# Kernel tuning notes

Measured on AMD Instinct MI355X. Metric: run time of the kernel, lower is better.

## Reference

```python
import jax, jax.numpy as jnp
import numpy as np

HIDDEN = 1024       # LUKE-large hidden size
NUM_HEADS = 16
NUM_ENTITIES = 42   # entities per doc (segment count)
EMBED = 768
BLOCK = 64
OUT_EMBED = 768
NUM_CLASS = 97
PROJ = 128
NEG_INF = -1e30


def setup_inputs() -> dict:
    key = jax.random.key(0)
    ks = jax.random.split(key, 16)
    B, L, M, R = 4, 1024, 128, 512
    s = 0.02
    return {
        "seq_lhs": jax.random.normal(ks[0], (B, L, HIDDEN), jnp.float32),
        "ent_lhs": jax.random.normal(ks[1], (B, M, HIDDEN), jnp.float32),
        "ent_to_seq_attn": jax.random.uniform(ks[2], (B, NUM_HEADS, M, L), jnp.float32),
        "entity_id_labels": jax.random.randint(ks[3], (B, M), 0, NUM_ENTITIES, jnp.int32),
        "hts": jax.random.randint(ks[4], (B, R, 2), 0, NUM_ENTITIES, jnp.int32),
        "W_head": jax.random.normal(ks[5], (2 * HIDDEN, EMBED), jnp.float32) * s,
        "b_head": jnp.zeros((EMBED,), jnp.float32),
        "W_tail": jax.random.normal(ks[6], (2 * HIDDEN, EMBED), jnp.float32) * s,
        "b_tail": jnp.zeros((EMBED,), jnp.float32),
        "W_bil": jax.random.normal(ks[7], (EMBED * BLOCK, OUT_EMBED), jnp.float32) * s,
        "b_bil": jnp.zeros((OUT_EMBED,), jnp.float32),
        "W_cls": jax.random.normal(ks[8], (OUT_EMBED, NUM_CLASS), jnp.float32) * s,
        "b_cls": jnp.zeros((NUM_CLASS,), jnp.float32),
        "W_proj": jax.random.normal(ks[9], (OUT_EMBED, PROJ), jnp.float32) * s,
        "b_proj": jnp.zeros((PROJ,), jnp.float32),
    }


def _pool_doc(seq, ent, attn, labels, ht):
    # seq [L,D], ent [M,D], attn [H,M,L], labels [M] int, ht [R,2] int
    onehot = (labels[None, :] == jnp.arange(NUM_ENTITIES)[:, None])  # [E,M]
    counts = onehot.sum(1)                                            # [E]
    # segment logsumexp over mentions (count==1 reduces to identity, matching torch)
    scores = jnp.where(onehot[:, :, None], ent[None, :, :], NEG_INF)  # [E,M,D]
    lse = jax.scipy.special.logsumexp(scores, axis=1)                 # [E,D]
    ent_emb = jnp.where(counts[:, None] > 0, lse, 0.0)                # zeros for empty entities
    # segment mean of attention over mentions: [E,H,L]
    oh = onehot.astype(attn.dtype)
    attn_sum = jnp.einsum('em,hml->ehl', oh, attn)
    attn_mean = attn_sum / jnp.maximum(counts, 1).astype(attn.dtype)[:, None, None]
    hs = ent_emb[ht[:, 0]]            # [R,D]
    ts = ent_emb[ht[:, 1]]            # [R,D]
    ha = attn_mean[ht[:, 0]]          # [R,H,L]
    ta = attn_mean[ht[:, 1]]          # [R,H,L]
    hta = (ha * ta).mean(1)           # [R,L]
    hta = hta / (hta.sum(1, keepdims=True) + 1e-5)
    rel = jnp.einsum('ld,rl->rd', seq, hta)  # [R,D]
    return hs, ts, rel


def reference(seq_lhs, ent_lhs, ent_to_seq_attn, entity_id_labels, hts,
              W_head, b_head, W_tail, b_tail, W_bil, b_bil, W_cls, b_cls, W_proj, b_proj):
    hs, ts, rel = jax.vmap(_pool_doc)(seq_lhs, ent_lhs, ent_to_seq_attn, entity_id_labels, hts)
    D = seq_lhs.shape[-1]
    hs = hs.reshape(-1, D)
    ts = ts.reshape(-1, D)
    rel = rel.reshape(-1, D)
    h = jnp.tanh(jnp.concatenate([hs, rel], axis=1) @ W_head + b_head)  # [N,EMBED]
    t = jnp.tanh(jnp.concatenate([ts, rel], axis=1) @ W_tail + b_tail)  # [N,EMBED]
    nb = EMBED // BLOCK
    b1 = h.reshape(-1, nb, BLOCK)
    b2 = t.reshape(-1, nb, BLOCK)
    bl = (b1[:, :, :, None] * b2[:, :, None, :]).reshape(-1, EMBED * BLOCK)
    embeds = bl @ W_bil + b_bil
    class_logits = embeds @ W_cls + b_cls
    proj_logits = jnp.tanh(embeds @ W_proj + b_proj)
    return embeds, class_logits, proj_logits
```

## Files before the change

### kernel.cpp

```cpp
#include <hip/hip_runtime.h>
#include <hip/hip_bf16.h>
#include <math.h>

#define BB   4
#define LL   1024
#define MM   128
#define RR   512
#define HID  1024
#define NH   16
#define NE   42
#define EMB  768
#define NBK  12
#define NC   97
#define PJ   128
#define NROWS 2048
#define KTOT (NBK * 4096)

typedef __attribute__((ext_vector_type(8))) short short8;
typedef __attribute__((ext_vector_type(4))) float floatx4;
typedef unsigned short ushort;

__device__ __forceinline__ float bf2f(ushort u) {
    return __uint_as_float(((unsigned int)u) << 16);
}
__device__ __forceinline__ ushort f2bf(float f) {
    __hip_bfloat16 h = __float2bfloat16(f);
    return *reinterpret_cast<ushort*>(&h);
}
__device__ __forceinline__ void async16(void* lds_base_uniform, const void* gsrc) {
    __builtin_amdgcn_global_load_lds(
        (const __attribute__((address_space(1))) unsigned int*)gsrc,
        (__attribute__((address_space(3))) unsigned int*)lds_base_uniform,
        16, 0, 0);
}
__device__ __forceinline__ void stage_w(short (*wlds)[4096], int bn,
                                        const ushort* wsrc, size_t t,
                                        int w, int lane) {
    const ushort* ts = wsrc + t * 4096;
    async16((void*)&wlds[bn][w * 512],        ts + w * 512 + lane * 8);
    async16((void*)&wlds[bn][2048 + w * 512], ts + 2048 + w * 512 + lane * 8);
}

__global__ __launch_bounds__(128) void k_members(const int* __restrict__ labels,
                                                 int* __restrict__ counts,
                                                 int* __restrict__ members) {
    int b = blockIdx.x;
    __shared__ int cnt[NE];
    int tid = threadIdx.x;
    if (tid < NE) cnt[tid] = 0;
    __syncthreads();
    if (tid < MM) {
        int lab = labels[b * MM + tid];
        int pos = atomicAdd(&cnt[lab], 1);
        members[(b * NE + lab) * MM + pos] = tid;
    }
    __syncthreads();
    if (tid < NE) counts[b * NE + tid] = cnt[tid];
}

__global__ __launch_bounds__(256) void k_entemb(const float* __restrict__ ent,
                                                const int* __restrict__ counts,
                                                const int* __restrict__ members,
                                                ushort* __restrict__ entbf) {
    int be = blockIdx.x;
    int b  = be / NE;
    int c  = counts[be];
    int tid = threadIdx.x;
    if (c == 0) {
#pragma unroll
        for (int u = 0; u < 4; ++u)
            entbf[(size_t)be * HID + tid + u * 256] = 0;
        return;
    }
    const int* mem = members + be * MM;
    const float* base = ent + (size_t)b * MM * HID;
#pragma unroll
    for (int u = 0; u < 4; ++u) {
        int d = tid + u * 256;
        float mx = -3.0e38f;
        for (int k = 0; k < c; ++k) {
            float x = base[(size_t)mem[k] * HID + d];
            mx = fmaxf(mx, x);
        }
        float s = 0.0f;
        for (int k = 0; k < c; ++k) {
            float x = base[(size_t)mem[k] * HID + d];
            s += expf(x - mx);
        }
        entbf[(size_t)be * HID + d] = f2bf(logf(s) + mx);
    }
}

__global__ __launch_bounds__(256) void k_attnmean(const float* __restrict__ attn,
                                                  const int* __restrict__ counts,
                                                  const int* __restrict__ members,
                                                  float* __restrict__ am) {
    int be = blockIdx.x;
    int hh = blockIdx.y;
    int b  = be / NE;
    int c  = counts[be];
    const int* mem = members + be * MM;
    float inv = 1.0f / (float)((c > 0) ? c : 1);
    const float* abase = attn + ((size_t)(b * NH + hh)) * MM * LL;
    int tid = threadIdx.x;
#pragma unroll
    for (int u = 0; u < 4; ++u) {
        int l = tid + u * 256;
        float s = 0.0f;
        for (int k = 0; k < c; ++k) s += abase[(size_t)mem[k] * LL + l];
        am[((size_t)be * NH + hh) * LL + l] = s * inv;
    }
}

__global__ __launch_bounds__(256) void k_hta(const float* __restrict__ am,
                                             const int* __restrict__ hts,
                                             ushort* __restrict__ htabf) {
    int br = blockIdx.x;
    int b  = br >> 9;
    int e0 = hts[br * 2 + 0];
    int e1 = hts[br * 2 + 1];
    const float* a0 = am + ((size_t)(b * NE + e0)) * NH * LL;
    const float* a1 = am + ((size_t)(b * NE + e1)) * NH * LL;
    int tid = threadIdx.x;
    float v[4] = {0.f, 0.f, 0.f, 0.f};
    for (int hh = 0; hh < NH; ++hh) {
        const float* p0 = a0 + hh * LL;
        const float* p1 = a1 + hh * LL;
#pragma unroll
        for (int u = 0; u < 4; ++u) {
            int l = tid + u * 256;
            v[u] = fmaf(p0[l], p1[l], v[u]);
        }
    }
    float part = 0.f;
#pragma unroll
    for (int u = 0; u < 4; ++u) { v[u] *= (1.0f / 16.0f); part += v[u]; }
    __shared__ float red[256];
    red[tid] = part;
    __syncthreads();
    for (int s = 128; s > 0; s >>= 1) {
        if (tid < s) red[tid] += red[tid + s];
        __syncthreads();
    }
    float scale = 1.0f / (red[0] + 1e-5f);
#pragma unroll
    for (int u = 0; u < 4; ++u)
        htabf[(size_t)br * LL + tid + u * 256] = f2bf(v[u] * scale);
}

__global__ __launch_bounds__(256) void k_prepB(const float* __restrict__ src,
                                               ushort* __restrict__ dst,
                                               int K, int N, long srcStride) {
    long flat = (long)blockIdx.x * 256 + threadIdx.x;
    int lane = (int)(flat & 63);
    long rest = flat >> 6;
    int cg = (int)(rest & 3); rest >>= 2;
    int NK0 = K >> 5;
    int k0 = (int)(rest % NK0); rest /= NK0;
    int NCB = N >> 6;
    int cb = (int)(rest % NCB);
    int bt = (int)(rest / NCB);
    int col = cb * 64 + cg * 16 + (lane & 15);
    int k   = k0 * 32 + (lane >> 4) * 8;
    const float* s = src + (size_t)bt * srcStride + (size_t)k * N + col;
    short8 out;
#pragma unroll
    for (int e = 0; e < 8; ++e)
        out[e] = (short)f2bf(s[(size_t)e * N]);
    *(short8*)(dst + (size_t)flat * 8) = out;
}

__global__ __launch_bounds__(256) void k_rel_mfma(const ushort* __restrict__ htabf,
                                                  const ushort* __restrict__ seqprep,
                                                  ushort* __restrict__ relbf) {
    __shared__ __align__(16) short wlds[2][4096];
    const int b = blockIdx.z;
    const int tid = threadIdx.x, lane = tid & 63, w = tid >> 6;
    const int lan16 = lane & 15, lgrp = lane >> 4;
    const int row0 = blockIdx.x * 128, cb = blockIdx.y, col0 = cb * 64;
    const ushort* wsrc = seqprep + ((size_t)b * 16 + cb) * 32 * 2048;
    const ushort* aP[2];
#pragma unroll
    for (int rg = 0; rg < 2; ++rg) {
        int r = row0 + w * 32 + rg * 16 + lan16;
        aP[rg] = htabf + ((size_t)b * RR + r) * LL;
    }
    floatx4 acc[2][4];
#pragma unroll
    for (int rg = 0; rg < 2; ++rg)
#pragma unroll
        for (int cg = 0; cg < 4; ++cg)
            acc[rg][cg] = (floatx4){0.f, 0.f, 0.f, 0.f};

    stage_w(wlds, 0, wsrc, 0, w, lane);
    __syncthreads();
    int buf = 0;
    for (int it = 0; it < 16; ++it) {
        short8 afr[2][2];
#pragma unroll
        for (int rg = 0; rg < 2; ++rg)
#pragma unroll
            for (int ks = 0; ks < 2; ++ks)
                afr[rg][ks] = *(const short8*)(aP[rg] + it * 64 + ks * 32 + lgrp * 8);
        if (it < 15) stage_w(wlds, buf ^ 1, wsrc, it + 1, w, lane);
#pragma unroll
        for (int ks = 0; ks < 2; ++ks) {
            short8 bfr[4];
#pragma unroll
            for (int cg = 0; cg < 4; ++cg)
                bfr[cg] = *(const short8*)&wlds[buf][ks * 2048 + cg * 512 + lane * 8];
#pragma unroll
            for (int rg = 0; rg < 2; ++rg)
#pragma unroll
                for (int cg = 0; cg < 4; ++cg)
                    acc[rg][cg] = __builtin_amdgcn_mfma_f32_16x16x32_bf16(
                        afr[rg][ks], bfr[cg], acc[rg][cg], 0, 0, 0);
        }
        __syncthreads();
        buf ^= 1;
    }
#pragma unroll
    for (int rg = 0; rg < 2; ++rg)
#pragma unroll
        for (int cg = 0; cg < 4; ++cg)
#pragma unroll
            for (int q = 0; q < 4; ++q) {
                int rr = row0 + w * 32 + rg * 16 + lgrp * 4 + q;
                int cc = col0 + cg * 16 + lan16;
                relbf[((size_t)b * RR + rr) * HID + cc] = f2bf(acc[rg][cg][q]);
            }
}

__global__ __launch_bounds__(256) void k_ht_mfma(const ushort* __restrict__ entbf,
                                                 const ushort* __restrict__ relbf,
                                                 const int* __restrict__ hts,
                                                 const ushort* __restrict__ wprepH,
                                                 const ushort* __restrict__ wprepT,
                                                 const float* __restrict__ bH,
                                                 const float* __restrict__ bT,
                                                 ushort* __restrict__ hT,
                                                 ushort* __restrict__ tbf) {
    __shared__ __align__(16) short wlds[2][4096];
    const int z = blockIdx.z;
    const ushort* wp  = z ? wprepT : wprepH;
    const float* bias = z ? bT : bH;
    const int tid = threadIdx.x, lane = tid & 63, w = tid >> 6;
    const int lan16 = lane & 15, lgrp = lane >> 4;
    const int row0 = blockIdx.x * 128, cb = blockIdx.y, col0 = cb * 64;
    const ushort* wsrc = wp + (size_t)cb * 64 * 2048;
    const ushort* aE[2];
    const ushort* aR[2];
#pragma unroll
    for (int rg = 0; rg < 2; ++rg) {
        int r = row0 + w * 32 + rg * 16 + lan16;
        int b = r >> 9, rr = r & 511;
        int e = hts[(b * RR + rr) * 2 + z];
        aE[rg] = entbf + (size_t)(b * NE + e) * HID;
        aR[rg] = relbf + (size_t)r * HID;
    }
    floatx4 acc[2][4];
#pragma unroll
    for (int rg = 0; rg < 2; ++rg)
#pragma unroll
        for (int cg = 0; cg < 4; ++cg)
            acc[rg][cg] = (floatx4){0.f, 0.f, 0.f, 0.f};

    stage_w(wlds, 0, wsrc, 0, w, lane);
    __syncthreads();
    int buf = 0;
    for (int it = 0; it < 32; ++it) {
        short8 afr[2][2];
        const int kb = (it < 16) ? it * 64 : it * 64 - 1024;
#pragma unroll
        for (int rg = 0; rg < 2; ++rg) {
            const ushort* ap = (it < 16 ? aE[rg] : aR[rg]) + kb + lgrp * 8;
#pragma unroll
            for (int ks = 0; ks < 2; ++ks)
                afr[rg][ks] = *(const short8*)(ap + ks * 32);
        }
        if (it < 31) stage_w(wlds, buf ^ 1, wsrc, it + 1, w, lane);
#pragma unroll
        for (int ks = 0; ks < 2; ++ks) {
            short8 bfr[4];
#pragma unroll
            for (int cg = 0; cg < 4; ++cg)
                bfr[cg] = *(const short8*)&wlds[buf][ks * 2048 + cg * 512 + lane * 8];
#pragma unroll
            for (int rg = 0; rg < 2; ++rg)
#pragma unroll
                for (int cg = 0; cg < 4; ++cg)
                    acc[rg][cg] = __builtin_amdgcn_mfma_f32_16x16x32_bf16(
                        afr[rg][ks], bfr[cg], acc[rg][cg], 0, 0, 0);
        }
        __syncthreads();
        buf ^= 1;
    }
#pragma unroll
    for (int rg = 0; rg < 2; ++rg)
#pragma unroll
        for (int cg = 0; cg < 4; ++cg)
#pragma unroll
            for (int q = 0; q < 4; ++q) {
                int rr = row0 + w * 32 + rg * 16 + lgrp * 4 + q;
                int cc = col0 + cg * 16 + lan16;
                ushort v = f2bf(tanhf(acc[rg][cg][q] + bias[cc]));
                if (z == 0) hT[(size_t)cc * NROWS + rr] = v;
                else        tbf[(size_t)rr * EMB + cc] = v;
            }
}

__global__ __launch_bounds__(256, 2) void k_bilinear(const ushort* __restrict__ hT,
                                                     const ushort* __restrict__ tbf,
                                                     const ushort* __restrict__ wprep,
                                                     float* __restrict__ partials) {
    __shared__ __align__(16) ushort h_lds[64 * 256];
    __shared__ __align__(16) short  wlds[2][4096];

    const int tid  = threadIdx.x;
    const int lane = tid & 63;
    const int w    = tid >> 6;
    const int lan16 = lane & 15;
    const int lgrp  = lane >> 4;
    const int rb = blockIdx.x, cb = blockIdx.y, zz = blockIdx.z;
    const int nb0 = zz * 3;
    const int row0 = rb * 256;
    const int col0 = cb * 64;
    const int rbase = w * 64;
    const ushort* wsrc = wprep + (size_t)((cb * 12 + nb0) * 64) * 4096;

    floatx4 acc[4][4];
#pragma unroll
    for (int rg = 0; rg < 4; ++rg)
#pragma unroll
        for (int cg = 0; cg < 4; ++cg)
            acc[rg][cg] = (floatx4){0.f, 0.f, 0.f, 0.f};

    stage_w(wlds, 0, wsrc, 0, w, lane);
    int buf = 0;
    for (int nbi = 0; nbi < 3; ++nbi) {
        const int nb = nb0 + nbi;
#pragma unroll
        for (int c = 0; c < 8; ++c) {
            void* dst = (void*)&h_lds[c * 2048 + w * 512];
            const ushort* src = hT + (size_t)(nb * 64 + c * 8 + w * 2 + (lane >> 5)) * NROWS
                                   + row0 + (lane & 31) * 8;
            async16(dst, src);
        }
        float tf[4][2][8];
#pragma unroll
        for (int rg = 0; rg < 4; ++rg)
#pragma unroll
            for (int ks = 0; ks < 2; ++ks) {
                const ushort* tp = tbf + (size_t)(row0 + rbase + rg * 16 + lan16) * EMB
                                       + nb * 64 + ks * 32 + lgrp * 8;
                short8 raw = *(const short8*)tp;
#pragma unroll
                for (int e = 0; e < 8; ++e)
                    tf[rg][ks][e] = bf2f((ushort)raw[e]);
            }
        __syncthreads();

        for (int i = 0; i < 64; ++i) {
            const int t = nbi * 64 + i;
            if (t < 191) stage_w(wlds, buf ^ 1, wsrc, t + 1, w, lane);
            float hv[4];
#pragma unroll
            for (int rg = 0; rg < 4; ++rg)
                hv[rg] = bf2f(h_lds[i * 256 + rbase + rg * 16 + lan16]);
#pragma unroll
            for (int ks = 0; ks < 2; ++ks) {
                short8 bfr[4];
#pragma unroll
                for (int cg = 0; cg < 4; ++cg)
                    bfr[cg] = *(const short8*)&wlds[buf][ks * 2048 + cg * 512 + lane * 8];
#pragma unroll
                for (int rg = 0; rg < 4; ++rg) {
                    short8 afr;
#pragma unroll
                    for (int e = 0; e < 8; ++e)
                        afr[e] = (short)f2bf(hv[rg] * tf[rg][ks][e]);
#pragma unroll
                    for (int cg = 0; cg < 4; ++cg)
                        acc[rg][cg] = __builtin_amdgcn_mfma_f32_16x16x32_bf16(
                            afr, bfr[cg], acc[rg][cg], 0, 0, 0);
                }
            }
            __syncthreads();
            buf ^= 1;
        }
    }

    float* pbase = partials + (size_t)zz * NROWS * EMB;
#pragma unroll
    for (int rg = 0; rg < 4; ++rg)
#pragma unroll
        for (int cg = 0; cg < 4; ++cg)
#pragma unroll
            for (int q = 0; q < 4; ++q)
                pbase[(size_t)(row0 + rbase + rg * 16 + lgrp * 4 + q) * EMB
                      + col0 + cg * 16 + lan16] = acc[rg][cg][q];
}

__global__ __launch_bounds__(256) void k_redbias(const float* __restrict__ partials,
                                                 const float* __restrict__ bias,
                                                 float* __restrict__ embeds) {
    int idx = blockIdx.x * 256 + threadIdx.x;
    const float4* p4 = (const float4*)partials;
    float4 s = p4[idx];
#pragma unroll
    for (int zz = 1; zz < 4; ++zz) {
        float4 v = p4[(size_t)zz * (NROWS * EMB / 4) + idx];
        s.x += v.x; s.y += v.y; s.z += v.z; s.w += v.w;
    }
    float4 b = ((const float4*)bias)[idx % (EMB / 4)];
    s.x += b.x; s.y += b.y; s.z += b.z; s.w += b.w;
    ((float4*)embeds)[idx] = s;
}

__global__ __launch_bounds__(256) void k_wcomb(const float* __restrict__ Wc,
                                               const float* __restrict__ Wp,
                                               float* __restrict__ Wcomb) {
    int k = blockIdx.x;
    int c = threadIdx.x;
    float v = (c < NC) ? Wc[(size_t)k * NC + c]
                       : ((c < NC + PJ) ? Wp[(size_t)k * PJ + (c - NC)] : 0.0f);
    Wcomb[(size_t)k * 256 + c] = v;
}

__global__ __launch_bounds__(256) void k_cls(const float* __restrict__ embeds,
                                             const float* __restrict__ Wcomb,
                                             const float* __restrict__ bc,
                                             const float* __restrict__ bp,
                                             float* __restrict__ cls_out,
                                             float* __restrict__ proj_out) {
    __shared__ float As[16][68];
    __shared__ float Bs[16][68];
    int tid = threadIdx.x;
    int tx = tid & 15, ty = tid >> 4;
    int row0 = blockIdx.x * 64, col0 = blockIdx.y * 64;
    float acc[4][4] = {};
    for (int k0 = 0; k0 < EMB; k0 += 16) {
        {
            int kk4 = (tid & 3) << 2, m = tid >> 2;
            float4 va = *(const float4*)&embeds[(size_t)(row0 + m) * EMB + k0 + kk4];
            As[kk4 + 0][m] = va.x; As[kk4 + 1][m] = va.y;
            As[kk4 + 2][m] = va.z; As[kk4 + 3][m] = va.w;
        }
        {
            int n4 = (tid & 15) << 2, kk = tid >> 4;
            float4 vb = *(const float4*)&Wcomb[(size_t)(k0 + kk) * 256 + col0 + n4];
            *(float4*)&Bs[kk][n4] = vb;
        }
        __syncthreads();
#pragma unroll
        for (int kk = 0; kk < 16; ++kk) {
            float4 a4 = *(const float4*)&As[kk][ty << 2];
            float4 b4 = *(const float4*)&Bs[kk][tx << 2];
            float av[4] = {a4.x, a4.y, a4.z, a4.w};
            float bv[4] = {b4.x, b4.y, b4.z, b4.w};
#pragma unroll
            for (int q = 0; q < 4; ++q)
#pragma unroll
                for (int p = 0; p < 4; ++p)
                    acc[q][p] = fmaf(av[q], bv[p], acc[q][p]);
        }
        __syncthreads();
    }
#pragma unroll
    for (int q = 0; q < 4; ++q)
#pragma unroll
        for (int p = 0; p < 4; ++p) {
            int c = col0 + (tx << 2) + p;
            int r = row0 + (ty << 2) + q;
            if (c < NC) {
                cls_out[(size_t)r * NC + c] = acc[q][p] + bc[c];
            } else if (c < NC + PJ) {
                int pp = c - NC;
                proj_out[(size_t)r * PJ + pp] = tanhf(acc[q][p] + bp[pp]);
            }
        }
}

extern "C" void kernel_launch(void* const* d_in, const int* in_sizes, int n_in,
                              void* d_out, int out_size, void* d_ws, size_t ws_size,
                              hipStream_t stream) {
    const float* seq    = (const float*)d_in[0];
    const float* ent    = (const float*)d_in[1];
    const float* attn   = (const float*)d_in[2];
    const int*   labels = (const int*)d_in[3];
    const int*   hts    = (const int*)d_in[4];
    const float* W_head = (const float*)d_in[5];
    const float* b_head = (const float*)d_in[6];
    const float* W_tail = (const float*)d_in[7];
    const float* b_tail = (const float*)d_in[8];
    const float* W_bil  = (const float*)d_in[9];
    const float* b_bil  = (const float*)d_in[10];
    const float* W_cls  = (const float*)d_in[11];
    const float* b_cls  = (const float*)d_in[12];
    const float* W_proj = (const float*)d_in[13];
    const float* b_proj = (const float*)d_in[14];

    char* p = (char*)d_ws;
    auto alloc = [&](size_t bytes) {
        void* r = (void*)p;
        p += (bytes + 255) & ~(size_t)255;
        return r;
    };
    int*    counts   = (int*)alloc(256 * 4);
    int*    members  = (int*)alloc((size_t)BB * NE * MM * 4);
    ushort* entbf    = (ushort*)alloc((size_t)BB * NE * HID * 2);
    float*  am       = (float*)alloc((size_t)BB * NE * NH * LL * 4);
    ushort* htabf    = (ushort*)alloc((size_t)BB * RR * LL * 2);
    ushort* relbf    = (ushort*)alloc((size_t)NROWS * HID * 2);
    ushort* hT       = (ushort*)alloc((size_t)EMB * NROWS * 2);
    ushort* tbf      = (ushort*)alloc((size_t)NROWS * EMB * 2);
    ushort* wprepBil = (ushort*)alloc((size_t)KTOT * EMB * 2);
    ushort* wprepH   = (ushort*)alloc((size_t)2 * HID * EMB * 2);
    ushort* wprepT   = (ushort*)alloc((size_t)2 * HID * EMB * 2);
    ushort* seqprep  = (ushort*)alloc((size_t)BB * LL * HID * 2);
    float*  Wcomb    = (float*)alloc((size_t)EMB * 256 * 4);
    float*  partials = (float*)alloc((size_t)4 * NROWS * EMB * 4);

    float* embeds_out = (float*)d_out;
    float* cls_out    = embeds_out + NROWS * EMB;
    float* proj_out   = cls_out + NROWS * NC;

    hipLaunchKernelGGL(k_prepB, dim3((size_t)KTOT * EMB / 8 / 256), dim3(256), 0, stream,
                       W_bil, wprepBil, KTOT, EMB, 0L);
    hipLaunchKernelGGL(k_prepB, dim3(2 * HID * EMB / 8 / 256), dim3(256), 0, stream,
                       W_head, wprepH, 2 * HID, EMB, 0L);
    hipLaunchKernelGGL(k_prepB, dim3(2 * HID * EMB / 8 / 256), dim3(256), 0, stream,
                       W_tail, wprepT, 2 * HID, EMB, 0L);
    hipLaunchKernelGGL(k_prepB, dim3(BB * LL * HID / 8 / 256), dim3(256), 0, stream,
                       seq, seqprep, LL, HID, (long)LL * HID);
    hipLaunchKernelGGL(k_wcomb, dim3(EMB), dim3(256), 0, stream,
                       W_cls, W_proj, Wcomb);

    hipLaunchKernelGGL(k_members, dim3(BB), dim3(128), 0, stream,
                       labels, counts, members);
    hipLaunchKernelGGL(k_entemb, dim3(BB * NE), dim3(256), 0, stream,
                       ent, counts, members, entbf);
    hipLaunchKernelGGL(k_attnmean, dim3(BB * NE, NH), dim3(256), 0, stream,
                       attn, counts, members, am);
    hipLaunchKernelGGL(k_hta, dim3(BB * RR), dim3(256), 0, stream,
                       am, hts, htabf);

    hipLaunchKernelGGL(k_rel_mfma, dim3(RR / 128, HID / 64, BB), dim3(256), 0, stream,
                       htabf, seqprep, relbf);
    hipLaunchKernelGGL(k_ht_mfma, dim3(NROWS / 128, EMB / 64, 2), dim3(256), 0, stream,
                       entbf, relbf, hts, wprepH, wprepT, b_head, b_tail, hT, tbf);
    hipLaunchKernelGGL(k_bilinear, dim3(NROWS / 256, EMB / 64, 4), dim3(256), 0, stream,
                       hT, tbf, wprepBil, partials);
    hipLaunchKernelGGL(k_redbias, dim3(NROWS * EMB / 4 / 256), dim3(256), 0, stream,
                       partials, b_bil, embeds_out);
    hipLaunchKernelGGL(k_cls, dim3(NROWS / 64, 4), dim3(256), 0, stream,
                       embeds_out, Wcomb, b_cls, b_proj, cls_out, proj_out);
}
```

Measured before the change: 702.3 us.

## Retile bilinear kernel to 128-row blocks with XCD-aware block mapping

Halves the row tile of the bilinear GEMM from 256 to 128, raising the grid from 384 to 768 blocks and the occupancy hint to 3 per CU. Blocks are remapped so those sharing a weight column block and K-split land on the same XCD, improving L2 reuse of the large W_bil stream. Weight staging now loads two K-steps per barrier to halve synchronisations. Smaller row tiles mean each weight tile is reused across fewer rows, so total weight traffic doubles and depends on the L2 locality gain.

```diff
diff --git a/kernel.cpp b/kernel.cpp
--- a/kernel.cpp
+++ b/kernel.cpp
@@ -309,46 +309,65 @@
             }
 }
 
-__global__ __launch_bounds__(256, 2) void k_bilinear(const ushort* __restrict__ hT,
+__global__ __launch_bounds__(256, 3) void k_bilinear(const ushort* __restrict__ hT,
                                                      const ushort* __restrict__ tbf,
                                                      const ushort* __restrict__ wprep,
                                                      float* __restrict__ partials) {
-    __shared__ __align__(16) ushort h_lds[64 * 256];
-    __shared__ __align__(16) short  wlds[2][4096];
+    __shared__ __align__(16) ushort h_lds[64 * 128];
+    __shared__ __align__(16) short  wlds[2][8192];
 
     const int tid  = threadIdx.x;
     const int lane = tid & 63;
     const int w    = tid >> 6;
     const int lan16 = lane & 15;
     const int lgrp  = lane >> 4;
-    const int rb = blockIdx.x, cb = blockIdx.y, zz = blockIdx.z;
+    const int L   = blockIdx.x;
+    const int xcd = L & 7;
+    const int t_  = L >> 3;
+    const int rb  = t_ & 15;
+    const int gq  = t_ >> 4;
+    const int g   = gq * 8 + xcd;
+    const int cb  = g >> 2;
+    const int zz  = g & 3;
     const int nb0 = zz * 3;
-    const int row0 = rb * 256;
+    const int row0 = rb * 128;
     const int col0 = cb * 64;
-    const int rbase = w * 64;
+    const int rbase = w * 32;
     const ushort* wsrc = wprep + (size_t)((cb * 12 + nb0) * 64) * 4096;
 
-    floatx4 acc[4][4];
-#pragma unroll
-    for (int rg = 0; rg < 4; ++rg)
+    auto stage_w2 = [&](int bn, int p) {
+        const ushort* ts = wsrc + (size_t)p * 8192;
+#pragma unroll
+        for (int s = 0; s < 4; ++s) {
+            int m = s * 4 + w;
+            async16((void*)&wlds[bn][m * 512], ts + m * 512 + lane * 8);
+        }
+    };
+    auto stage_h = [&](int nb) {
+#pragma unroll
+        for (int s = 0; s < 4; ++s) {
+            int m = s * 4 + w;
+            async16((void*)&h_lds[m * 512],
+                    hT + (size_t)(nb * 64 + m * 4 + (lane >> 4)) * NROWS
+                       + row0 + lan16 * 8);
+        }
+    };
+
+    floatx4 acc[2][4];
+#pragma unroll
+    for (int rg = 0; rg < 2; ++rg)
 #pragma unroll
         for (int cg = 0; cg < 4; ++cg)
             acc[rg][cg] = (floatx4){0.f, 0.f, 0.f, 0.f};
 
-    stage_w(wlds, 0, wsrc, 0, w, lane);
+    stage_w2(0, 0);
     int buf = 0;
     for (int nbi = 0; nbi < 3; ++nbi) {
         const int nb = nb0 + nbi;
-#pragma unroll
-        for (int c = 0; c < 8; ++c) {
-            void* dst = (void*)&h_lds[c * 2048 + w * 512];
-            const ushort* src = hT + (size_t)(nb * 64 + c * 8 + w * 2 + (lane >> 5)) * NROWS
-                                   + row0 + (lane & 31) * 8;
-            async16(dst, src);
-        }
-        float tf[4][2][8];
-#pragma unroll
-        for (int rg = 0; rg < 4; ++rg)
+        stage_h(nb);
+        float tf[2][2][8];
+#pragma unroll
+        for (int rg = 0; rg < 2; ++rg)
 #pragma unroll
             for (int ks = 0; ks < 2; ++ks) {
                 const ushort* tp = tbf + (size_t)(row0 + rbase + rg * 16 + lan16) * EMB
@@ -360,29 +379,34 @@
             }
         __syncthreads();
 
-        for (int i = 0; i < 64; ++i) {
-            const int t = nbi * 64 + i;
-            if (t < 191) stage_w(wlds, buf ^ 1, wsrc, t + 1, w, lane);
-            float hv[4];
-#pragma unroll
-            for (int rg = 0; rg < 4; ++rg)
-                hv[rg] = bf2f(h_lds[i * 256 + rbase + rg * 16 + lan16]);
-#pragma unroll
-            for (int ks = 0; ks < 2; ++ks) {
-                short8 bfr[4];
-#pragma unroll
-                for (int cg = 0; cg < 4; ++cg)
-                    bfr[cg] = *(const short8*)&wlds[buf][ks * 2048 + cg * 512 + lane * 8];
-#pragma unroll
-                for (int rg = 0; rg < 4; ++rg) {
-                    short8 afr;
-#pragma unroll
-                    for (int e = 0; e < 8; ++e)
-                        afr[e] = (short)f2bf(hv[rg] * tf[rg][ks][e]);
+        for (int p = 0; p < 32; ++p) {
+            const int pp = nbi * 32 + p;
+            if (pp < 95) stage_w2(buf ^ 1, pp + 1);
+#pragma unroll
+            for (int ii = 0; ii < 2; ++ii) {
+                const int i = p * 2 + ii;
+                float hv[2];
+#pragma unroll
+                for (int rg = 0; rg < 2; ++rg)
+                    hv[rg] = bf2f(h_lds[i * 128 + rbase + rg * 16 + lan16]);
+#pragma unroll
+                for (int ks = 0; ks < 2; ++ks) {
+                    short8 bfr[4];
 #pragma unroll
                     for (int cg = 0; cg < 4; ++cg)
-                        acc[rg][cg] = __builtin_amdgcn_mfma_f32_16x16x32_bf16(
-                            afr, bfr[cg], acc[rg][cg], 0, 0, 0);
+                        bfr[cg] = *(const short8*)&wlds[buf][ii * 4096 + ks * 2048
+                                                            + cg * 512 + lane * 8];
+#pragma unroll
+                    for (int rg = 0; rg < 2; ++rg) {
+                        short8 afr;
+#pragma unroll
+                        for (int e = 0; e < 8; ++e)
+                            afr[e] = (short)f2bf(hv[rg] * tf[rg][ks][e]);
+#pragma unroll
+                        for (int cg = 0; cg < 4; ++cg)
+                            acc[rg][cg] = __builtin_amdgcn_mfma_f32_16x16x32_bf16(
+                                afr, bfr[cg], acc[rg][cg], 0, 0, 0);
+                    }
                 }
             }
             __syncthreads();
@@ -392,7 +416,7 @@
 
     float* pbase = partials + (size_t)zz * NROWS * EMB;
 #pragma unroll
-    for (int rg = 0; rg < 4; ++rg)
+    for (int rg = 0; rg < 2; ++rg)
 #pragma unroll
         for (int cg = 0; cg < 4; ++cg)
 #pragma unroll
@@ -549,7 +573,7 @@
                        htabf, seqprep, relbf);
     hipLaunchKernelGGL(k_ht_mfma, dim3(NROWS / 128, EMB / 64, 2), dim3(256), 0, stream,
                        entbf, relbf, hts, wprepH, wprepT, b_head, b_tail, hT, tbf);
-    hipLaunchKernelGGL(k_bilinear, dim3(NROWS / 256, EMB / 64, 4), dim3(256), 0, stream,
+    hipLaunchKernelGGL(k_bilinear, dim3(768), dim3(256), 0, stream,
                        hT, tbf, wprepBil, partials);
     hipLaunchKernelGGL(k_redbias, dim3(NROWS * EMB / 4 / 256), dim3(256), 0, stream,
                        partials, b_bil, embeds_out);
```

Measured after the change: 635.1 us. -9.6%, faster.
